# Kernel optimization log

Hardware: AMD Instinct MI355X
Metric: run time of the kernel (lower is better)

The kernel has to match this reference:

```python
import jax, jax.numpy as jnp
import numpy as np

LN_EPS = 1e-5
Q_EPS = 1e-5


def ternary_quantize(w):
    # BitNet b1.58-style: scale by mean(|W|), round, clip to {-1, 0, 1}
    scale = jnp.mean(jnp.abs(w))
    return jnp.clip(jnp.round(w / (scale + Q_EPS)), -1.0, 1.0)


def layernorm(x, gamma, beta):
    mu = jnp.mean(x, axis=-1, keepdims=True)
    var = jnp.mean(jnp.square(x - mu), axis=-1, keepdims=True)
    return (x - mu) * jax.lax.rsqrt(var + LN_EPS) * gamma + beta


def setup_inputs() -> dict:
    key = jax.random.key(0)
    k_x, k_w = jax.random.split(key)
    B, S, D_IN, D_OUT = 4, 2048, 2048, 2048
    x = jax.random.normal(k_x, (B, S, D_IN), dtype=jnp.float32)
    # kaiming_normal_ fan_out, relu: std = sqrt(2 / fan_out) = sqrt(2 / out_features)
    std = np.sqrt(2.0 / D_OUT).astype(np.float32)
    weight = jax.random.normal(k_w, (D_OUT, D_IN), dtype=jnp.float32) * std
    bias = jnp.zeros((D_OUT,), dtype=jnp.float32)
    ln_gamma = jnp.ones((D_IN,), dtype=jnp.float32)
    ln_beta = jnp.zeros((D_IN,), dtype=jnp.float32)
    return {"x": x, "weight": weight, "bias": bias, "ln_gamma": ln_gamma, "ln_beta": ln_beta}


def reference(x, weight, bias, ln_gamma, ln_beta):
    xn = layernorm(x, ln_gamma, ln_beta)          # [B, S, D_in]
    w_q = ternary_quantize(weight)                 # [D_out, D_in] in {-1, 0, 1}
    return jnp.einsum('bsi,oi->bso', xn, w_q) + bias
```

## Files before the change

kernel.cpp:

```cpp
#include <hip/hip_runtime.h>
#include <hip/hip_bf16.h>

#define D_IN  2048
#define D_OUT 2048
#define M_TOTAL 8192

typedef __attribute__((ext_vector_type(4))) int   i32x4;
typedef __attribute__((ext_vector_type(4))) float f32x4;

typedef const __attribute__((address_space(1))) void gvoid_t;
typedef __attribute__((address_space(3))) void lvoid_t;

__global__ __launch_bounds__(256) void absum_kernel(const float* __restrict__ w,
                                                    double* __restrict__ partials) {
    const int n4 = (D_OUT * D_IN) / 4;
    int tid = blockIdx.x * 256 + threadIdx.x;
    int stride = gridDim.x * 256;
    double s = 0.0;
    for (int i = tid; i < n4; i += stride) {
        float4 v = reinterpret_cast<const float4*>(w)[i];
        s += (double)fabsf(v.x) + (double)fabsf(v.y) +
             (double)fabsf(v.z) + (double)fabsf(v.w);
    }
    for (int off = 32; off; off >>= 1) s += __shfl_xor(s, off, 64);
    __shared__ double ls[4];
    if ((threadIdx.x & 63) == 0) ls[threadIdx.x >> 6] = s;
    __syncthreads();
    if (threadIdx.x == 0)
        partials[blockIdx.x] = ls[0] + ls[1] + ls[2] + ls[3];
}

__device__ __forceinline__ unsigned pk4(float a, float b, float c, float d, float is) {
    int q0 = (int)rintf(a * is); q0 = min(127, max(-127, q0));
    int q1 = (int)rintf(b * is); q1 = min(127, max(-127, q1));
    int q2 = (int)rintf(c * is); q2 = min(127, max(-127, q2));
    int q3 = (int)rintf(d * is); q3 = min(127, max(-127, q3));
    return  (unsigned)(unsigned char)(char)q0        |
           ((unsigned)(unsigned char)(char)q1 << 8)  |
           ((unsigned)(unsigned char)(char)q2 << 16) |
           ((unsigned)(unsigned char)(char)q3 << 24);
}

__global__ __launch_bounds__(256) void quantln_kernel(const float* __restrict__ w,
                                                      const double* __restrict__ partials,
                                                      char* __restrict__ wq,
                                                      const float* __restrict__ x,
                                                      const float* __restrict__ gamma,
                                                      const float* __restrict__ beta,
                                                      char* __restrict__ xn,
                                                      float* __restrict__ s_row) {
    int t = threadIdx.x;
    if (blockIdx.x < 4096) {
        double s = partials[t] + partials[t + 256] + partials[t + 512] + partials[t + 768];
        for (int off = 32; off; off >>= 1) s += __shfl_xor(s, off, 64);
        __shared__ double ls[4];
        if ((t & 63) == 0) ls[t >> 6] = s;
        __syncthreads();
        double tot = ls[0] + ls[1] + ls[2] + ls[3];
        double inv = 1.0 / (tot / 4194304.0 + 1e-5);

        int i = blockIdx.x * 256 + t;
        float4 v = reinterpret_cast<const float4*>(w)[i];
        unsigned o = 0;
        #pragma unroll
        for (int j = 0; j < 4; ++j) {
            float wf = (j == 0) ? v.x : (j == 1) ? v.y : (j == 2) ? v.z : v.w;
            double r = rint((double)wf * inv);
            r = fmin(1.0, fmax(-1.0, r));
            int q = (int)r;
            o |= ((unsigned)(unsigned char)(char)q) << (8 * j);
        }
        reinterpret_cast<unsigned*>(wq)[i] = o;
    } else {
        int row = blockIdx.x - 4096;
        const float4* xr = reinterpret_cast<const float4*>(x + (size_t)row * D_IN);
        float4 v0 = xr[t];
        float4 v1 = xr[t + 256];
        float s  = v0.x + v0.y + v0.z + v0.w + v1.x + v1.y + v1.z + v1.w;
        float sq = v0.x*v0.x + v0.y*v0.y + v0.z*v0.z + v0.w*v0.w
                 + v1.x*v1.x + v1.y*v1.y + v1.z*v1.z + v1.w*v1.w;
        for (int off = 32; off; off >>= 1) {
            s  += __shfl_xor(s,  off, 64);
            sq += __shfl_xor(sq, off, 64);
        }
        __shared__ float lss[4], lqq[4], lmx[4];
        if ((t & 63) == 0) { lss[t >> 6] = s; lqq[t >> 6] = sq; }
        __syncthreads();
        s  = lss[0] + lss[1] + lss[2] + lss[3];
        sq = lqq[0] + lqq[1] + lqq[2] + lqq[3];
        float mu  = s * (1.0f / D_IN);
        float var = sq * (1.0f / D_IN) - mu * mu;
        float inv = rsqrtf(var + 1e-5f);

        const float4* g4 = reinterpret_cast<const float4*>(gamma);
        const float4* b4 = reinterpret_cast<const float4*>(beta);
        float4 g0 = g4[t], g1 = g4[t + 256];
        float4 b0 = b4[t], b1 = b4[t + 256];

        float a0 = (v0.x - mu) * inv * g0.x + b0.x;
        float a1 = (v0.y - mu) * inv * g0.y + b0.y;
        float a2 = (v0.z - mu) * inv * g0.z + b0.z;
        float a3 = (v0.w - mu) * inv * g0.w + b0.w;
        float a4 = (v1.x - mu) * inv * g1.x + b1.x;
        float a5 = (v1.y - mu) * inv * g1.y + b1.y;
        float a6 = (v1.z - mu) * inv * g1.z + b1.z;
        float a7 = (v1.w - mu) * inv * g1.w + b1.w;

        float mx = fmaxf(fmaxf(fmaxf(fabsf(a0), fabsf(a1)), fmaxf(fabsf(a2), fabsf(a3))),
                         fmaxf(fmaxf(fabsf(a4), fabsf(a5)), fmaxf(fabsf(a6), fabsf(a7))));
        for (int off = 32; off; off >>= 1) mx = fmaxf(mx, __shfl_xor(mx, off, 64));
        if ((t & 63) == 0) lmx[t >> 6] = mx;
        __syncthreads();
        float rowmax = fmaxf(fmaxf(lmx[0], lmx[1]), fmaxf(lmx[2], lmx[3]));

        float is = (rowmax > 0.0f) ? (127.0f / rowmax) : 0.0f;
        char* orow = xn + (size_t)row * D_IN;
        reinterpret_cast<unsigned*>(orow)[t]        = pk4(a0, a1, a2, a3, is);
        reinterpret_cast<unsigned*>(orow + 1024)[t] = pk4(a4, a5, a6, a7, is);
        if (t == 0) s_row[row] = rowmax * (1.0f / 127.0f);
    }
}

#define BM 256
#define BN 256
#define NT (D_IN / 64)

__device__ __forceinline__ void stage_quantum(const char* __restrict__ gbase,
                                              int grow0, int kcol0,
                                              char* smem, int ldsbase, int tid) {
    const int lane = tid & 63;
    const int w    = tid >> 6;
    const int colx = (((lane & 3) ^ ((lane >> 3) & 3)) << 4);
    #pragma unroll
    for (int j = 0; j < 2; ++j) {
        const int c = w * 2 + j;
        const int r = c * 16 + (lane >> 2);
        const char* g = gbase + (size_t)(grow0 + r) * D_IN + kcol0 + colx;
        char* l = smem + ldsbase + c * 1024 + lane * 16;
        __builtin_amdgcn_global_load_lds((gvoid_t*)g, (lvoid_t*)l, 16, 0, 0);
    }
}

__device__ __forceinline__ i32x4 rdfrag(const char* smem, int off) {
    return *reinterpret_cast<const i32x4*>(smem + off);
}

template<int W>
__device__ __forceinline__ void vm_wait() {
    if constexpr (W == 4) {
        asm volatile("s_waitcnt vmcnt(4)" ::: "memory");
        __builtin_amdgcn_sched_barrier(0);
    } else if constexpr (W == 0) {
        asm volatile("s_waitcnt vmcnt(0)" ::: "memory");
        __builtin_amdgcn_sched_barrier(0);
    }
}

#define MFMA16(ROW, AV, BV)                                                     \
    _Pragma("unroll")                                                           \
    for (int m_ = 0; m_ < 4; ++m_)                                              \
        _Pragma("unroll")                                                       \
        for (int n_ = 0; n_ < 4; ++n_)                                          \
            acc[ROW + m_][n_] = __builtin_amdgcn_mfma_i32_16x16x64_i8(          \
                AV[m_], BV[n_], acc[ROW + m_][n_], 0, 0, 0);

template<int W, bool S, bool RD>
__device__ __forceinline__ void ktile(int T,
        const char* __restrict__ A, const char* __restrict__ B,
        int bm, int bn, char* smem, int tid, int aBase, int bBase,
        i32x4 (&aS0)[4], i32x4 (&aS1)[4], i32x4 (&bCur)[4], i32x4 (&bNxt)[4],
        i32x4 (&acc)[8][4]) {
    const int sA  = ((T & 3) << 14);
    const int sAn = (((T + 1) & 3) << 14);

    #pragma unroll
    for (int f = 0; f < 4; ++f) aS1[f] = rdfrag(smem, sA + aBase + 4096 + f * 1024);
    MFMA16(0, aS0, bCur)
    vm_wait<W>();
    asm volatile("s_barrier" ::: "memory");

    if (RD) {
        #pragma unroll
        for (int f = 0; f < 4; ++f) aS0[f]  = rdfrag(smem, sAn + aBase + f * 1024);
        #pragma unroll
        for (int f = 0; f < 4; ++f) bNxt[f] = rdfrag(smem, 65536 + sAn + bBase + f * 1024);
    }
    if (S) {
        const int s3 = (((T + 3) & 3) << 14);
        stage_quantum(A, bm, (T + 3) * 64, smem, s3,         tid);
        stage_quantum(B, bn, (T + 3) * 64, smem, 65536 + s3, tid);
    }
    MFMA16(4, aS1, bCur)
}

__global__ __launch_bounds__(512, 2) void gemm256_kernel(const char* __restrict__ A,
                                                         const char* __restrict__ B,
                                                         const float* __restrict__ bias,
                                                         const float* __restrict__ s_row,
                                                         float* __restrict__ C) {
    extern __shared__ char smem[];
    const int tid  = threadIdx.x;
    const int lane = tid & 63;
    const int wid  = tid >> 6;
    const int wm   = wid >> 2;
    const int wn   = wid & 3;

    const int orig = blockIdx.y * gridDim.x + blockIdx.x;
    const int swz  = (orig & 7) * 32 + (orig >> 3);
    const int bm   = (swz >> 3) * BM;
    const int bn   = (swz & 7) * BN;

    const int lr   = lane & 15;
    const int rdbase = lr * 64 + ((((lane >> 4) ^ ((lr >> 1) & 3))) << 4);
    const int aBase = wm * 8192 + rdbase;
    const int bBase = wn * 4096 + rdbase;

    i32x4 acc[8][4];
    #pragma unroll
    for (int m = 0; m < 8; ++m)
        #pragma unroll
        for (int n = 0; n < 4; ++n)
            acc[m][n] = (i32x4){0, 0, 0, 0};

    i32x4 aS0[4], aS1[4], bE[4], bO[4];

    stage_quantum(A, bm, 0,   smem, 0,             tid);
    stage_quantum(B, bn, 0,   smem, 65536,         tid);
    stage_quantum(A, bm, 64,  smem, 16384,         tid);
    stage_quantum(B, bn, 64,  smem, 65536 + 16384, tid);
    stage_quantum(A, bm, 128, smem, 32768,         tid);
    stage_quantum(B, bn, 128, smem, 65536 + 32768, tid);
    asm volatile("s_waitcnt vmcnt(8)" ::: "memory");
    __builtin_amdgcn_sched_barrier(0);
    asm volatile("s_barrier" ::: "memory");
    #pragma unroll
    for (int f = 0; f < 4; ++f) aS0[f] = rdfrag(smem, aBase + f * 1024);
    #pragma unroll
    for (int f = 0; f < 4; ++f) bE[f]  = rdfrag(smem, 65536 + bBase + f * 1024);

    for (int T = 0; T < 28; T += 2) {
        ktile<4, true, true>(T,     A, B, bm, bn, smem, tid, aBase, bBase, aS0, aS1, bE, bO, acc);
        ktile<4, true, true>(T + 1, A, B, bm, bn, smem, tid, aBase, bBase, aS0, aS1, bO, bE, acc);
    }
    ktile<4,  true,  true >(28, A, B, bm, bn, smem, tid, aBase, bBase, aS0, aS1, bE, bO, acc);
    ktile<4,  false, true >(29, A, B, bm, bn, smem, tid, aBase, bBase, aS0, aS1, bO, bE, acc);
    ktile<0,  false, true >(30, A, B, bm, bn, smem, tid, aBase, bBase, aS0, aS1, bE, bO, acc);
    ktile<-1, false, false>(31, A, B, bm, bn, smem, tid, aBase, bBase, aS0, aS1, bO, bE, acc);

    asm volatile("s_barrier" ::: "memory");

    const int EST = 272;
    char* eb = smem + wid * (16 * EST);
    const int C0 = bn + wn * 64;
    const int R0 = bm + wm * 128;
    const int rowsub = (lane >> 4) * 4;
    float bv[4];
    #pragma unroll
    for (int n = 0; n < 4; ++n) bv[n] = bias[C0 + n * 16 + lr];

    #pragma unroll
    for (int m = 0; m < 8; ++m) {
        float sr[4];
        #pragma unroll
        for (int i = 0; i < 4; ++i) sr[i] = s_row[R0 + m * 16 + rowsub + i];
        #pragma unroll
        for (int n = 0; n < 4; ++n)
            #pragma unroll
            for (int i = 0; i < 4; ++i)
                *reinterpret_cast<float*>(eb + (rowsub + i) * EST + (n * 16 + lr) * 4)
                    = (float)acc[m][n][i] * sr[i] + bv[n];
        #pragma unroll
        for (int q = 0; q < 4; ++q) {
            const int row = (lane >> 4) + q * 4;
            f32x4 v = *reinterpret_cast<const f32x4*>(eb + row * EST + lr * 16);
            *reinterpret_cast<f32x4*>(&C[(size_t)(R0 + m * 16 + row) * D_OUT + C0 + lr * 4]) = v;
        }
    }
}

extern "C" void kernel_launch(void* const* d_in, const int* in_sizes, int n_in,
                              void* d_out, int out_size, void* d_ws, size_t ws_size,
                              hipStream_t stream) {
    const float* x     = (const float*)d_in[0];
    const float* w     = (const float*)d_in[1];
    const float* bias  = (const float*)d_in[2];
    const float* gamma = (const float*)d_in[3];
    const float* beta  = (const float*)d_in[4];
    float* out = (float*)d_out;

    char* ws = (char*)d_ws;
    double* partials = (double*)ws;
    float*  s_row    = (float*)(ws + 8192);
    char*   wq       = ws + 65536;
    char*   xn       = ws + 65536 + 4ull * 1024 * 1024;

    hipFuncSetAttribute(reinterpret_cast<const void*>(gemm256_kernel),
                        hipFuncAttributeMaxDynamicSharedMemorySize, 131072);

    absum_kernel   <<<1024, 256, 0, stream>>>(w, partials);
    quantln_kernel <<<12288, 256, 0, stream>>>(w, partials, wq, x, gamma, beta, xn, s_row);
    gemm256_kernel <<<dim3(D_OUT / BN, M_TOTAL / BM), 512, 131072, stream>>>(xn, wq, bias, s_row, out);
}
```

Baseline: 63.23 us.

## Load B fragments directly from global into registers, bypassing LDS staging

The weight operand B is no longer staged through shared memory with global_load_lds. Each wave now reads its B fragments straight from global memory into registers one k-tile ahead, while only A keeps the LDS ring. This halves dynamic LDS to 64 KB and cuts the staging traffic and LDS reads for B. In exchange, each wave issues its own narrow, strided global loads, and waves that share columns duplicate them. The compiler may also insert conservative vmcnt waits that stall the MFMA pipeline.

```diff
diff --git a/kernel.cpp b/kernel.cpp
--- a/kernel.cpp
+++ b/kernel.cpp
@@ -150,6 +150,9 @@
     if constexpr (W == 4) {
         asm volatile("s_waitcnt vmcnt(4)" ::: "memory");
         __builtin_amdgcn_sched_barrier(0);
+    } else if constexpr (W == 2) {
+        asm volatile("s_waitcnt vmcnt(2)" ::: "memory");
+        __builtin_amdgcn_sched_barrier(0);
     } else if constexpr (W == 0) {
         asm volatile("s_waitcnt vmcnt(0)" ::: "memory");
         __builtin_amdgcn_sched_barrier(0);
@@ -166,8 +169,8 @@
 
 template<int W, bool S, bool RD>
 __device__ __forceinline__ void ktile(int T,
-        const char* __restrict__ A, const char* __restrict__ B,
-        int bm, int bn, char* smem, int tid, int aBase, int bBase,
+        const char* __restrict__ A, const char* __restrict__ Bw,
+        int bm, char* smem, int tid, int aBase, int bRow, int bKsub,
         i32x4 (&aS0)[4], i32x4 (&aS1)[4], i32x4 (&bCur)[4], i32x4 (&bNxt)[4],
         i32x4 (&acc)[8][4]) {
     const int sA  = ((T & 3) << 14);
@@ -181,14 +184,15 @@
 
     if (RD) {
         #pragma unroll
-        for (int f = 0; f < 4; ++f) aS0[f]  = rdfrag(smem, sAn + aBase + f * 1024);
-        #pragma unroll
-        for (int f = 0; f < 4; ++f) bNxt[f] = rdfrag(smem, 65536 + sAn + bBase + f * 1024);
+        for (int f = 0; f < 4; ++f) aS0[f] = rdfrag(smem, sAn + aBase + f * 1024);
+        const size_t kb = (size_t)(T + 1) * 64 + bKsub;
+        #pragma unroll
+        for (int f = 0; f < 4; ++f)
+            bNxt[f] = *reinterpret_cast<const i32x4*>(Bw + (size_t)(bRow + f * 16) * D_IN + kb);
     }
     if (S) {
         const int s3 = (((T + 3) & 3) << 14);
-        stage_quantum(A, bm, (T + 3) * 64, smem, s3,         tid);
-        stage_quantum(B, bn, (T + 3) * 64, smem, 65536 + s3, tid);
+        stage_quantum(A, bm, (T + 3) * 64, smem, s3, tid);
     }
     MFMA16(4, aS1, bCur)
 }
@@ -213,7 +217,8 @@
     const int lr   = lane & 15;
     const int rdbase = lr * 64 + ((((lane >> 4) ^ ((lr >> 1) & 3))) << 4);
     const int aBase = wm * 8192 + rdbase;
-    const int bBase = wn * 4096 + rdbase;
+    const int bRow  = bn + wn * 64 + lr;
+    const int bKsub = (lane >> 4) << 4;
 
     i32x4 acc[8][4];
     #pragma unroll
@@ -224,28 +229,26 @@
 
     i32x4 aS0[4], aS1[4], bE[4], bO[4];
 
-    stage_quantum(A, bm, 0,   smem, 0,             tid);
-    stage_quantum(B, bn, 0,   smem, 65536,         tid);
-    stage_quantum(A, bm, 64,  smem, 16384,         tid);
-    stage_quantum(B, bn, 64,  smem, 65536 + 16384, tid);
-    stage_quantum(A, bm, 128, smem, 32768,         tid);
-    stage_quantum(B, bn, 128, smem, 65536 + 32768, tid);
-    asm volatile("s_waitcnt vmcnt(8)" ::: "memory");
+    stage_quantum(A, bm, 0,   smem, 0,     tid);
+    stage_quantum(A, bm, 64,  smem, 16384, tid);
+    stage_quantum(A, bm, 128, smem, 32768, tid);
+    asm volatile("s_waitcnt vmcnt(4)" ::: "memory");
     __builtin_amdgcn_sched_barrier(0);
     asm volatile("s_barrier" ::: "memory");
     #pragma unroll
     for (int f = 0; f < 4; ++f) aS0[f] = rdfrag(smem, aBase + f * 1024);
     #pragma unroll
-    for (int f = 0; f < 4; ++f) bE[f]  = rdfrag(smem, 65536 + bBase + f * 1024);
+    for (int f = 0; f < 4; ++f)
+        bE[f] = *reinterpret_cast<const i32x4*>(B + (size_t)(bRow + f * 16) * D_IN + bKsub);
 
     for (int T = 0; T < 28; T += 2) {
-        ktile<4, true, true>(T,     A, B, bm, bn, smem, tid, aBase, bBase, aS0, aS1, bE, bO, acc);
-        ktile<4, true, true>(T + 1, A, B, bm, bn, smem, tid, aBase, bBase, aS0, aS1, bO, bE, acc);
-    }
-    ktile<4,  true,  true >(28, A, B, bm, bn, smem, tid, aBase, bBase, aS0, aS1, bE, bO, acc);
-    ktile<4,  false, true >(29, A, B, bm, bn, smem, tid, aBase, bBase, aS0, aS1, bO, bE, acc);
-    ktile<0,  false, true >(30, A, B, bm, bn, smem, tid, aBase, bBase, aS0, aS1, bE, bO, acc);
-    ktile<-1, false, false>(31, A, B, bm, bn, smem, tid, aBase, bBase, aS0, aS1, bO, bE, acc);
+        ktile<2, true, true>(T,     A, B, bm, smem, tid, aBase, bRow, bKsub, aS0, aS1, bE, bO, acc);
+        ktile<2, true, true>(T + 1, A, B, bm, smem, tid, aBase, bRow, bKsub, aS0, aS1, bO, bE, acc);
+    }
+    ktile<2,  true,  true >(28, A, B, bm, smem, tid, aBase, bRow, bKsub, aS0, aS1, bE, bO, acc);
+    ktile<2,  false, true >(29, A, B, bm, smem, tid, aBase, bRow, bKsub, aS0, aS1, bO, bE, acc);
+    ktile<0,  false, true >(30, A, B, bm, smem, tid, aBase, bRow, bKsub, aS0, aS1, bE, bO, acc);
+    ktile<-1, false, false>(31, A, B, bm, smem, tid, aBase, bRow, bKsub, aS0, aS1, bO, bE, acc);
 
     asm volatile("s_barrier" ::: "memory");
 
@@ -295,9 +298,9 @@
     char*   xn       = ws + 65536 + 4ull * 1024 * 1024;
 
     hipFuncSetAttribute(reinterpret_cast<const void*>(gemm256_kernel),
-                        hipFuncAttributeMaxDynamicSharedMemorySize, 131072);
+                        hipFuncAttributeMaxDynamicSharedMemorySize, 65536);
 
     absum_kernel   <<<1024, 256, 0, stream>>>(w, partials);
     quantln_kernel <<<12288, 256, 0, stream>>>(w, partials, wq, x, gamma, beta, xn, s_row);
-    gemm256_kernel <<<dim3(D_OUT / BN, M_TOTAL / BM), 512, 131072, stream>>>(xn, wq, bias, s_row, out);
-}
+    gemm256_kernel <<<dim3(D_OUT / BN, M_TOTAL / BM), 512, 65536, stream>>>(xn, wq, bias, s_row, out);
+}
```

New measurement: 81.74 us. 1.29x slower.
